# Performance work log

Measured on AMD Instinct MI355X. Metric: run time of the kernel, lower is better.

## Reference

```python
import math
import jax, jax.numpy as jnp
import numpy as np

B, S, D, H = 2, 2048, 1024, 16
HD = D // H  # 64


def setup_inputs() -> dict:
    key = jax.random.key(0)
    k0, k1, k2, k3, k4 = jax.random.split(key, 5)
    x = jax.random.normal(k0, (B, S, D), dtype=jnp.float32)
    # standard RoPE angles: rotations[s, i] = (cos(s*theta_i), sin(s*theta_i))
    inv_freq = 1.0 / (10000.0 ** (jnp.arange(0, HD, 2, dtype=jnp.float32) / HD))  # [HD/2]
    ang = jnp.arange(S, dtype=jnp.float32)[:, None] * inv_freq[None, :]           # [S, HD/2]
    rotations = jnp.stack([jnp.cos(ang), jnp.sin(ang)], axis=-1)                  # [S, HD/2, 2]
    scale = D ** -0.5
    w_qkv = jax.random.normal(k1, (3 * D, D), dtype=jnp.float32) * scale
    b_qkv = jax.random.normal(k2, (3 * D,), dtype=jnp.float32) * 0.01
    w_o = jax.random.normal(k3, (D, D), dtype=jnp.float32) * scale
    b_o = jax.random.normal(k4, (D,), dtype=jnp.float32) * 0.01
    return {"input": x, "rotations": rotations, "w_qkv": w_qkv, "b_qkv": b_qkv,
            "w_o": w_o, "b_o": b_o}


def _apply_rotary(t, cos, sin):
    # t: [B, H, S, HD]; cos/sin: [S, HD/2] broadcast over B,H
    te, to = t[..., 0::2], t[..., 1::2]
    re = te * cos - to * sin
    ro = te * sin + to * cos
    return jnp.stack([re, ro], axis=-1).reshape(t.shape)


def reference(input, rotations, w_qkv, b_qkv, w_o, b_o):
    Bx, Sx, Dx = input.shape
    qkv = input @ w_qkv.T + b_qkv                      # [B, S, 3D]
    q, k, v = jnp.split(qkv, 3, axis=-1)
    def to_heads(t):
        return t.reshape(Bx, Sx, H, HD).transpose(0, 2, 1, 3)  # [B, H, S, HD]
    q, k, v = to_heads(q), to_heads(k), to_heads(v)
    cos, sin = rotations[..., 0], rotations[..., 1]    # [S, HD/2]
    q = _apply_rotary(q, cos, sin)
    k = _apply_rotary(k, cos, sin)
    scale = math.sqrt(1.0 / float(HD))
    scores = jnp.einsum('bhsd,bhtd->bhst', q * scale, k)  # [B, H, S, S]
    w = jax.nn.softmax(scores.astype(jnp.float32), axis=-1).astype(scores.dtype)
    attn = jnp.einsum('bhst,bhtd->bhsd', w, v)          # [B, H, S, HD]
    attn = attn.transpose(0, 2, 1, 3).reshape(Bx, Sx, Dx)
    return attn @ w_o.T + b_o
```

## Files before the change

kernel.cpp:

```cpp
#include <hip/hip_runtime.h>

typedef __bf16 bf16_t;
typedef __bf16 bf16x8 __attribute__((ext_vector_type(8)));
typedef __bf16 bf16x4 __attribute__((ext_vector_type(4)));
typedef __bf16 bf16x2 __attribute__((ext_vector_type(2)));
typedef float f32x4 __attribute__((ext_vector_type(4)));
typedef float f32x16 __attribute__((ext_vector_type(16)));

#define B_ 2
#define S_ 2048
#define D_ 1024
#define H_ 16
#define HD_ 64

#define MFMA(a, b, c) __builtin_amdgcn_mfma_f32_16x16x32_bf16(a, b, c, 0, 0, 0)
#define MFMA32(a, b, c) __builtin_amdgcn_mfma_f32_32x32x16_bf16(a, b, c, 0, 0, 0)

static __device__ __forceinline__ bf16x8 ldb8(const bf16_t* p) {
    return *(const bf16x8*)p;
}

static __device__ __forceinline__ void gload16(const void* g, void* l) {
    __builtin_amdgcn_global_load_lds((const __attribute__((address_space(1))) void*)g,
                                     (__attribute__((address_space(3))) void*)l, 16, 0, 0);
}

static __device__ __forceinline__ unsigned cvtpk(float a, float b) {
    union { bf16x2 h; unsigned u; } cv;
    cv.h[0] = (bf16_t)a;
    cv.h[1] = (bf16_t)b;
    return cv.u;
}
static __device__ __forceinline__ float xhalf_max(float x) {
    return fmaxf(x, __shfl_xor(x, 32));
}

__global__ __launch_bounds__(256) void k_cvt(const float* __restrict__ in,
                                             bf16_t* __restrict__ out, int n4) {
    int i = blockIdx.x * 256 + threadIdx.x;
    int stride = gridDim.x * 256;
    for (; i < n4; i += stride) {
        float4 v = ((const float4*)in)[i];
        bf16x4 o;
        o[0] = (bf16_t)v.x; o[1] = (bf16_t)v.y; o[2] = (bf16_t)v.z; o[3] = (bf16_t)v.w;
        ((bf16x4*)out)[i] = o;
    }
}

static __device__ __forceinline__ void gemm_core(const bf16_t* __restrict__ A,
                                                 const bf16_t* __restrict__ Bt,
                                                 const int K, bf16_t* ldsA, bf16_t* ldsB,
                                                 f32x4 acc[4][4]) {
    const int tid = threadIdx.x;
    const int wave = tid >> 6, lane = tid & 63;
    const int g = lane >> 4, q16 = lane & 15;
    const int wm = wave >> 1, wn = wave & 1;
    const int mb = blockIdx.x * 128, nb = blockIdx.y * 128;
    const int r0 = lane >> 2, c8 = (lane & 3) * 8;

#pragma unroll
    for (int i = 0; i < 4; ++i)
#pragma unroll
        for (int j = 0; j < 4; ++j) {
            f32x4 z = {0.f, 0.f, 0.f, 0.f};
            acc[i][j] = z;
        }

    const bf16_t* ga0 = A + (size_t)(mb + wave * 16 + r0) * K + c8;
    const bf16_t* ga1 = A + (size_t)(mb + 64 + wave * 16 + r0) * K + c8;
    const bf16_t* gb0 = Bt + (size_t)(nb + wave * 16 + r0) * K + c8;
    const bf16_t* gb1 = Bt + (size_t)(nb + 64 + wave * 16 + r0) * K + c8;
    bf16_t* la0 = ldsA + (wave * 16) * 32;
    bf16_t* la1 = ldsA + (64 + wave * 16) * 32;
    bf16_t* lb0 = ldsB + (wave * 16) * 32;
    bf16_t* lb1 = ldsB + (64 + wave * 16) * 32;

    for (int k0 = 0; k0 < K; k0 += 32) {
        gload16(ga0 + k0, la0);
        gload16(ga1 + k0, la1);
        gload16(gb0 + k0, lb0);
        gload16(gb1 + k0, lb1);
        __syncthreads();
        bf16x8 af[4], bfv[4];
#pragma unroll
        for (int i = 0; i < 4; ++i)
            af[i] = ldb8(ldsA + (wm * 64 + i * 16 + q16) * 32 + 8 * g);
#pragma unroll
        for (int j = 0; j < 4; ++j)
            bfv[j] = ldb8(ldsB + (wn * 64 + j * 16 + q16) * 32 + 8 * g);
#pragma unroll
        for (int i = 0; i < 4; ++i)
#pragma unroll
            for (int j = 0; j < 4; ++j)
                acc[i][j] = MFMA(af[i], bfv[j], acc[i][j]);
        __syncthreads();
    }
}

__global__ __launch_bounds__(256) void k_gemm_qkv(const bf16_t* __restrict__ xb,
                                                  const bf16_t* __restrict__ wqb,
                                                  const float* __restrict__ bqkv,
                                                  const float* __restrict__ rot,
                                                  bf16_t* __restrict__ qa,
                                                  bf16_t* __restrict__ kt,
                                                  bf16_t* __restrict__ vt) {
    __shared__ bf16_t ldsA[128 * 32];
    __shared__ bf16_t ldsB[128 * 32];
    f32x4 acc[4][4];
    gemm_core(xb, wqb, 1024, ldsA, ldsB, acc);

    const int tid = threadIdx.x;
    const int wave = tid >> 6, lane = tid & 63;
    const int g = lane >> 4, q16 = lane & 15;
    const int wm = wave >> 1, wn = wave & 1;
    const int mb = blockIdx.x * 128, nb = blockIdx.y * 128;
    const int third = nb >> 10;
    const float QS = 0.125f * 1.44269504088896f;

    if (third < 2) {
        const float2* cs2 = (const float2*)rot;
#pragma unroll
        for (int j = 0; j < 4; ++j) {
            int n = nb + wn * 64 + j * 16 + q16;
            float bias = bqkv[n];
            int d = n & 1023;
            int h = d >> 6, hd = d & 63;
            int i2 = hd >> 1;
            bool odd = (hd & 1) != 0;
#pragma unroll
            for (int i = 0; i < 4; ++i) {
                int m0 = mb + wm * 64 + i * 16 + 4 * g;
#pragma unroll
                for (int r = 0; r < 4; ++r) {
                    int mm = m0 + r;
                    int s = mm & 2047, b = mm >> 11;
                    float val = acc[i][j][r] + bias;
                    float prt = __shfl_xor(val, 1);
                    float2 cs = cs2[s * 32 + i2];
                    float rv = val * cs.x + (odd ? prt * cs.y : -(prt * cs.y));
                    size_t base = (size_t)(b * H_ + h) * (S_ * 64);
                    if (third == 0) {
                        qa[base + (size_t)s * HD_ + hd] = (bf16_t)(rv * QS);
                    } else {
                        int idx = ((s >> 5) << 11) + ((hd >> 4) << 9) + ((s & 31) << 4)
                                + (((hd >> 3) & 1) << 3) + (hd & 7);
                        kt[base + idx] = (bf16_t)rv;
                    }
                }
            }
        }
    } else {
#pragma unroll
        for (int j = 0; j < 4; ++j) {
            int n = nb + wn * 64 + j * 16 + q16;
            float bias = bqkv[n];
            int d = n & 1023;
            int h = d >> 6, hd = d & 63;
#pragma unroll
            for (int i = 0; i < 4; ++i) {
                int m0 = mb + wm * 64 + i * 16 + 4 * g;
                int s0 = m0 & 2047, b = m0 >> 11;
                bf16x4 pk;
#pragma unroll
                for (int r = 0; r < 4; ++r) pk[r] = (bf16_t)(acc[i][j][r] + bias);
                int x = (((s0 >> 4) & 1) << 1) + (hd >> 5);
                size_t base = (size_t)(b * H_ + h) * (S_ * 64);
                size_t idx = ((size_t)(s0 >> 5) << 11) + (x << 9) + ((hd & 31) << 4)
                           + (((s0 >> 3) & 1) << 3) + (s0 & 7);
                *(bf16x4*)(vt + base + idx) = pk;
            }
        }
    }
}

static __device__ __forceinline__ void loadK(const bf16_t* kbase, bf16x8 (&kf)[4]) {
#pragma unroll
    for (int j = 0; j < 4; ++j) kf[j] = ldb8(kbase + 512 * j);
}
static __device__ __forceinline__ void loadV(const bf16_t* vbase, bf16x8 (&vf)[4]) {
    vf[0] = ldb8(vbase);
    vf[1] = ldb8(vbase + 512);
    vf[2] = ldb8(vbase + 1024);
    vf[3] = ldb8(vbase + 1536);
}

static __device__ __forceinline__ f32x16 qk4(const bf16x8 (&kf)[4], const bf16x8 (&qf)[4]) {
    f32x16 s = {0.f, 0.f, 0.f, 0.f, 0.f, 0.f, 0.f, 0.f,
                0.f, 0.f, 0.f, 0.f, 0.f, 0.f, 0.f, 0.f};
    __builtin_amdgcn_s_setprio(1);
#pragma unroll
    for (int j = 0; j < 4; ++j) s = MFMA32(kf[j], qf[j], s);
    __builtin_amdgcn_s_setprio(0);
    return s;
}

static __device__ __forceinline__ void softmax_pa(f32x16& s, float& m, float& lsum,
                                                  f32x16& o0, f32x16& o1,
                                                  int hi, bf16x8& pa0v, bf16x8& pa1v) {
    float a0 = fmaxf(fmaxf(s[0], s[1]), s[2]);
    float a1 = fmaxf(fmaxf(s[3], s[4]), s[5]);
    float a2 = fmaxf(fmaxf(s[6], s[7]), s[8]);
    float a3 = fmaxf(fmaxf(s[9], s[10]), s[11]);
    float a4 = fmaxf(fmaxf(s[12], s[13]), s[14]);
    float tm = fmaxf(fmaxf(fmaxf(a0, a1), a2), fmaxf(fmaxf(a3, a4), s[15]));
    tm = xhalf_max(tm);

    bool ok = (tm <= m + 8.0f);
    if (!__all(ok)) {
        float mn = fmaxf(m, tm);
        float ce = __builtin_amdgcn_exp2f(m - mn);
        m = mn;
        lsum *= ce;
#pragma unroll
        for (int r = 0; r < 16; ++r) {
            int q = (r & 3) + 8 * (r >> 2) + 4 * hi;
            float c = __shfl(ce, q);
            o0[r] *= c; o1[r] *= c;
        }
    }

#pragma unroll
    for (int r = 0; r < 16; ++r) s[r] = __builtin_amdgcn_exp2f(s[r] - m);
    float ps = (((s[0] + s[1]) + (s[2] + s[3])) + ((s[4] + s[5]) + (s[6] + s[7])))
             + (((s[8] + s[9]) + (s[10] + s[11])) + ((s[12] + s[13]) + (s[14] + s[15])));
    lsum += ps;

    unsigned c0 = cvtpk(s[0], s[1]),   c1 = cvtpk(s[2], s[3]);
    unsigned c2 = cvtpk(s[4], s[5]),   c3 = cvtpk(s[6], s[7]);
    unsigned d0 = cvtpk(s[8], s[9]),   d1 = cvtpk(s[10], s[11]);
    unsigned d2 = cvtpk(s[12], s[13]), d3 = cvtpk(s[14], s[15]);
    unsigned x0 = __shfl_xor(c0, 32), x1 = __shfl_xor(c1, 32);
    unsigned x2 = __shfl_xor(c2, 32), x3 = __shfl_xor(c3, 32);
    unsigned y0 = __shfl_xor(d0, 32), y1 = __shfl_xor(d1, 32);
    unsigned y2 = __shfl_xor(d2, 32), y3 = __shfl_xor(d3, 32);

    union { unsigned u[4]; bf16x8 v; } pa0, pa1;
    pa0.u[0] = hi ? x2 : c0;
    pa0.u[1] = hi ? x3 : c1;
    pa0.u[2] = hi ? c2 : x0;
    pa0.u[3] = hi ? c3 : x1;
    pa1.u[0] = hi ? y2 : d0;
    pa1.u[1] = hi ? y3 : d1;
    pa1.u[2] = hi ? d2 : y0;
    pa1.u[3] = hi ? d3 : y1;
    pa0v = pa0.v;
    pa1v = pa1.v;
}

static __device__ __forceinline__ void pv4(const bf16x8 pa0, const bf16x8 pa1,
                                           const bf16x8 (&vf)[4], f32x16& o0, f32x16& o1) {
    __builtin_amdgcn_s_setprio(1);
    o0 = MFMA32(pa0, vf[0], o0);
    o1 = MFMA32(pa0, vf[1], o1);
    o0 = MFMA32(pa1, vf[2], o0);
    o1 = MFMA32(pa1, vf[3], o1);
    __builtin_amdgcn_s_setprio(0);
}

__global__ __launch_bounds__(256, 4) void k_attn(const bf16_t* __restrict__ qa,
                                                 const bf16_t* __restrict__ kt,
                                                 const bf16_t* __restrict__ vt,
                                                 bf16_t* __restrict__ attn) {
    __shared__ float lm[2][32];
    __shared__ float ll[2][32];
    __shared__ float lo[2][2][16][64];
    const int tid = threadIdx.x;
    const int wave = tid >> 6, lane = tid & 63;
    const int l31 = lane & 31, hi = lane >> 5;
    const int pair = wave & 1;
    const int thalf = wave >> 1;
    const int bh = blockIdx.y;
    const int q0 = blockIdx.x * 64 + pair * 32;

    const bf16_t* Qp = qa + ((size_t)bh * S_ + q0) * HD_;
    const int laneoff = (2 * l31 + hi) * 8;
    const bf16_t* kl = kt + (size_t)bh * (S_ * 64) + (size_t)thalf * 65536 + laneoff;
    const bf16_t* vl = vt + (size_t)bh * (S_ * 64) + (size_t)thalf * 65536 + laneoff;

    bf16x8 qf[4];
    const bf16_t* qptr = Qp + l31 * HD_ + 8 * hi;
#pragma unroll
    for (int j = 0; j < 4; ++j) qf[j] = ldb8(qptr + 16 * j);

    f32x16 o0 = {0.f, 0.f, 0.f, 0.f, 0.f, 0.f, 0.f, 0.f,
                 0.f, 0.f, 0.f, 0.f, 0.f, 0.f, 0.f, 0.f};
    f32x16 o1 = o0;
    float m = -1e30f, lsum = 0.f;

    bf16x8 kE[4], kO[4];
    loadK(kl, kE);

    for (int i = 0; i < 16; ++i) {
        {
            f32x16 s = qk4(kE, qf);
            loadK(kl + 2048, kO);
            bf16x8 vv[4];
            loadV(vl, vv);
            bf16x8 pa0, pa1;
            softmax_pa(s, m, lsum, o0, o1, hi, pa0, pa1);
            pv4(pa0, pa1, vv, o0, o1);
        }
        {
            f32x16 s = qk4(kO, qf);
            loadK(kl + 4096, kE);
            bf16x8 vv[4];
            loadV(vl + 2048, vv);
            bf16x8 pa0, pa1;
            softmax_pa(s, m, lsum, o0, o1, hi, pa0, pa1);
            pv4(pa0, pa1, vv, o0, o1);
        }
        kl += 4096;
        vl += 4096;
    }

    float lfull = lsum + __shfl_xor(lsum, 32);
    if (thalf) {
        if (!hi) {
            lm[pair][l31] = m;
            ll[pair][l31] = lfull;
        }
#pragma unroll
        for (int r = 0; r < 16; ++r) {
            lo[pair][0][r][lane] = o0[r];
            lo[pair][1][r][lane] = o1[r];
        }
    }
    __syncthreads();
    if (!thalf) {
        float mb_ = lm[pair][l31];
        float lb_ = ll[pair][l31];
        float ms = fmaxf(m, mb_);
        float ca = __builtin_amdgcn_exp2f(m - ms);
        float cb = __builtin_amdgcn_exp2f(mb_ - ms);
        float invL = 1.0f / (lfull * ca + lb_ * cb);
        const int b = bh >> 4, h = bh & 15;
        bf16_t* op = attn + ((size_t)b * S_ + q0) * D_ + h * HD_;
#pragma unroll
        for (int r = 0; r < 16; ++r) {
            int q = (r & 3) + 8 * (r >> 2) + 4 * hi;
            float caq = __shfl(ca, q);
            float cbq = __shfl(cb, q);
            float invq = __shfl(invL, q);
            float O0 = (o0[r] * caq + lo[pair][0][r][lane] * cbq) * invq;
            float O1 = (o1[r] * caq + lo[pair][1][r][lane] * cbq) * invq;
            op[(size_t)q * D_ + l31] = (bf16_t)O0;
            op[(size_t)q * D_ + 32 + l31] = (bf16_t)O1;
        }
    }
}

__global__ __launch_bounds__(256) void k_gemm_out(const bf16_t* __restrict__ attn,
                                                  const bf16_t* __restrict__ wob,
                                                  const float* __restrict__ bo,
                                                  float* __restrict__ out) {
    __shared__ bf16_t ldsA[128 * 32];
    __shared__ bf16_t ldsB[128 * 32];
    f32x4 acc[4][4];
    gemm_core(attn, wob, 1024, ldsA, ldsB, acc);

    const int tid = threadIdx.x;
    const int wave = tid >> 6, lane = tid & 63;
    const int g = lane >> 4, q16 = lane & 15;
    const int wm = wave >> 1, wn = wave & 1;
    const int mb = blockIdx.x * 128, nb = blockIdx.y * 128;
#pragma unroll
    for (int j = 0; j < 4; ++j) {
        int n = nb + wn * 64 + j * 16 + q16;
        float bias = bo[n];
#pragma unroll
        for (int i = 0; i < 4; ++i) {
            int m0 = mb + wm * 64 + i * 16 + 4 * g;
#pragma unroll
            for (int r = 0; r < 4; ++r)
                out[(size_t)(m0 + r) * D_ + n] = acc[i][j][r] + bias;
        }
    }
}

extern "C" void kernel_launch(void* const* d_in, const int* in_sizes, int n_in,
                              void* d_out, int out_size, void* d_ws, size_t ws_size,
                              hipStream_t stream) {
    const float* x    = (const float*)d_in[0];
    const float* rot  = (const float*)d_in[1];
    const float* wqkv = (const float*)d_in[2];
    const float* bqkv = (const float*)d_in[3];
    const float* wo   = (const float*)d_in[4];
    const float* bo   = (const float*)d_in[5];
    float* out = (float*)d_out;

    char* ws = (char*)d_ws;
    bf16_t* xb   = (bf16_t*)(ws);
    bf16_t* wqb  = (bf16_t*)(ws + ((size_t)8 << 20));
    bf16_t* wob  = (bf16_t*)(ws + ((size_t)14 << 20));
    bf16_t* qa   = (bf16_t*)(ws + ((size_t)16 << 20));
    bf16_t* kt   = (bf16_t*)(ws + ((size_t)24 << 20));
    bf16_t* vt   = (bf16_t*)(ws + ((size_t)32 << 20));
    bf16_t* attn = (bf16_t*)(ws + ((size_t)40 << 20));

    k_cvt<<<1024, 256, 0, stream>>>(x, xb, (B_ * S_ * D_) / 4);
    k_cvt<<<1024, 256, 0, stream>>>(wqkv, wqb, (3 * D_ * D_) / 4);
    k_cvt<<<1024, 256, 0, stream>>>(wo, wob, (D_ * D_) / 4);
    k_gemm_qkv<<<dim3(32, 24), 256, 0, stream>>>(xb, wqb, bqkv, rot, qa, kt, vt);
    k_attn<<<dim3(32, 32), 256, 0, stream>>>(qa, kt, vt, attn);
    k_gemm_out<<<dim3(32, 8), 256, 0, stream>>>(attn, wob, bo, out);
}
```

Before: 221.5 us.

## Merge conversion kernels and transpose Q/K GEMM for vectorized RoPE epilogue

The three fp32-to-bf16 conversion launches are merged into one kernel that picks its source buffer by index range, which removes two launches. For the Q and K sections of the QKV projection, the GEMM operands are swapped so each lane's accumulator holds four consecutive head-dim values for one token. RoPE rotation pairs therefore sit in the same lane, which removes the cross-lane shuffles and allows vectorized bias, rotation and bf16x4 stores in place of scalar scattered stores. The risks are extra branching in the conversion loop and a different GEMM memory access pattern for the swapped operands.

```diff
diff --git a/kernel.cpp b/kernel.cpp
--- a/kernel.cpp
+++ b/kernel.cpp
@@ -35,27 +35,43 @@
     return fmaxf(x, __shfl_xor(x, 32));
 }
 
-__global__ __launch_bounds__(256) void k_cvt(const float* __restrict__ in,
-                                             bf16_t* __restrict__ out, int n4) {
+#define N4_X  1048576
+#define N4_WQ 786432
+#define N4_WO 262144
+__global__ __launch_bounds__(256) void k_cvt3(const float* __restrict__ x,
+                                              const float* __restrict__ wq,
+                                              const float* __restrict__ wo,
+                                              bf16_t* __restrict__ xb,
+                                              bf16_t* __restrict__ wqb,
+                                              bf16_t* __restrict__ wob) {
     int i = blockIdx.x * 256 + threadIdx.x;
     int stride = gridDim.x * 256;
-    for (; i < n4; i += stride) {
-        float4 v = ((const float4*)in)[i];
+    for (; i < N4_X + N4_WQ + N4_WO; i += stride) {
+        const float4* src;
+        bf16x4* dst;
+        int off;
+        if (i < N4_X) {
+            src = (const float4*)x; dst = (bf16x4*)xb; off = i;
+        } else if (i < N4_X + N4_WQ) {
+            src = (const float4*)wq; dst = (bf16x4*)wqb; off = i - N4_X;
+        } else {
+            src = (const float4*)wo; dst = (bf16x4*)wob; off = i - (N4_X + N4_WQ);
+        }
+        float4 v = src[off];
         bf16x4 o;
         o[0] = (bf16_t)v.x; o[1] = (bf16_t)v.y; o[2] = (bf16_t)v.z; o[3] = (bf16_t)v.w;
-        ((bf16x4*)out)[i] = o;
+        dst[off] = o;
     }
 }
 
 static __device__ __forceinline__ void gemm_core(const bf16_t* __restrict__ A,
                                                  const bf16_t* __restrict__ Bt,
                                                  const int K, bf16_t* ldsA, bf16_t* ldsB,
-                                                 f32x4 acc[4][4]) {
+                                                 f32x4 acc[4][4], int mb, int nb) {
     const int tid = threadIdx.x;
     const int wave = tid >> 6, lane = tid & 63;
     const int g = lane >> 4, q16 = lane & 15;
     const int wm = wave >> 1, wn = wave & 1;
-    const int mb = blockIdx.x * 128, nb = blockIdx.y * 128;
     const int r0 = lane >> 2, c8 = (lane & 3) * 8;
 
 #pragma unroll
@@ -106,59 +122,58 @@
                                                   bf16_t* __restrict__ vt) {
     __shared__ bf16_t ldsA[128 * 32];
     __shared__ bf16_t ldsB[128 * 32];
-    f32x4 acc[4][4];
-    gemm_core(xb, wqb, 1024, ldsA, ldsB, acc);
-
     const int tid = threadIdx.x;
     const int wave = tid >> 6, lane = tid & 63;
     const int g = lane >> 4, q16 = lane & 15;
     const int wm = wave >> 1, wn = wave & 1;
-    const int mb = blockIdx.x * 128, nb = blockIdx.y * 128;
-    const int third = nb >> 10;
+    const int sx = blockIdx.x;
+    const int third = blockIdx.y >> 3;
+    const int ny = blockIdx.y & 7;
     const float QS = 0.125f * 1.44269504088896f;
+    f32x4 acc[4][4];
 
     if (third < 2) {
-        const float2* cs2 = (const float2*)rot;
+        gemm_core(wqb, xb, 1024, ldsA, ldsB, acc, third * 1024 + ny * 128, sx * 128);
+        const int h = ny * 2 + wm;
+#pragma unroll
+        for (int i = 0; i < 4; ++i) {
+            const int hdb = i * 16 + 4 * g;
+            float4 bi = *(const float4*)&bqkv[third * 1024 + ny * 128 + wm * 64 + hdb];
+#pragma unroll
+            for (int j = 0; j < 4; ++j) {
+                int mm = sx * 128 + wn * 64 + j * 16 + q16;
+                int s = mm & 2047, b = mm >> 11;
+                float4 cs = *(const float4*)&rot[s * 64 + hdb];
+                float v0 = acc[i][j][0] + bi.x, v1 = acc[i][j][1] + bi.y;
+                float v2 = acc[i][j][2] + bi.z, v3 = acc[i][j][3] + bi.w;
+                float r0 = v0 * cs.x - v1 * cs.y, r1 = v0 * cs.y + v1 * cs.x;
+                float r2 = v2 * cs.z - v3 * cs.w, r3 = v2 * cs.w + v3 * cs.z;
+                size_t base = (size_t)(b * H_ + h) * (S_ * 64);
+                bf16x4 pk;
+                if (third == 0) {
+                    pk[0] = (bf16_t)(r0 * QS); pk[1] = (bf16_t)(r1 * QS);
+                    pk[2] = (bf16_t)(r2 * QS); pk[3] = (bf16_t)(r3 * QS);
+                    *(bf16x4*)(qa + base + (size_t)s * HD_ + hdb) = pk;
+                } else {
+                    pk[0] = (bf16_t)r0; pk[1] = (bf16_t)r1;
+                    pk[2] = (bf16_t)r2; pk[3] = (bf16_t)r3;
+                    size_t idx = ((size_t)(s >> 5) << 11) + (i << 9) + ((s & 31) << 4)
+                               + ((g >> 1) << 3) + ((g & 1) << 2);
+                    *(bf16x4*)(kt + base + idx) = pk;
+                }
+            }
+        }
+    } else {
+        gemm_core(xb, wqb, 1024, ldsA, ldsB, acc, sx * 128, 2048 + ny * 128);
 #pragma unroll
         for (int j = 0; j < 4; ++j) {
-            int n = nb + wn * 64 + j * 16 + q16;
+            int n = 2048 + ny * 128 + wn * 64 + j * 16 + q16;
             float bias = bqkv[n];
             int d = n & 1023;
             int h = d >> 6, hd = d & 63;
-            int i2 = hd >> 1;
-            bool odd = (hd & 1) != 0;
 #pragma unroll
             for (int i = 0; i < 4; ++i) {
-                int m0 = mb + wm * 64 + i * 16 + 4 * g;
-#pragma unroll
-                for (int r = 0; r < 4; ++r) {
-                    int mm = m0 + r;
-                    int s = mm & 2047, b = mm >> 11;
-                    float val = acc[i][j][r] + bias;
-                    float prt = __shfl_xor(val, 1);
-                    float2 cs = cs2[s * 32 + i2];
-                    float rv = val * cs.x + (odd ? prt * cs.y : -(prt * cs.y));
-                    size_t base = (size_t)(b * H_ + h) * (S_ * 64);
-                    if (third == 0) {
-                        qa[base + (size_t)s * HD_ + hd] = (bf16_t)(rv * QS);
-                    } else {
-                        int idx = ((s >> 5) << 11) + ((hd >> 4) << 9) + ((s & 31) << 4)
-                                + (((hd >> 3) & 1) << 3) + (hd & 7);
-                        kt[base + idx] = (bf16_t)rv;
-                    }
-                }
-            }
-        }
-    } else {
-#pragma unroll
-        for (int j = 0; j < 4; ++j) {
-            int n = nb + wn * 64 + j * 16 + q16;
-            float bias = bqkv[n];
-            int d = n & 1023;
-            int h = d >> 6, hd = d & 63;
-#pragma unroll
-            for (int i = 0; i < 4; ++i) {
-                int m0 = mb + wm * 64 + i * 16 + 4 * g;
+                int m0 = sx * 128 + wm * 64 + i * 16 + 4 * g;
                 int s0 = m0 & 2047, b = m0 >> 11;
                 bf16x4 pk;
 #pragma unroll
@@ -356,7 +371,7 @@
     __shared__ bf16_t ldsA[128 * 32];
     __shared__ bf16_t ldsB[128 * 32];
     f32x4 acc[4][4];
-    gemm_core(attn, wob, 1024, ldsA, ldsB, acc);
+    gemm_core(attn, wob, 1024, ldsA, ldsB, acc, blockIdx.x * 128, blockIdx.y * 128);
 
     const int tid = threadIdx.x;
     const int wave = tid >> 6, lane = tid & 63;
@@ -397,9 +412,7 @@
     bf16_t* vt   = (bf16_t*)(ws + ((size_t)32 << 20));
     bf16_t* attn = (bf16_t*)(ws + ((size_t)40 << 20));
 
-    k_cvt<<<1024, 256, 0, stream>>>(x, xb, (B_ * S_ * D_) / 4);
-    k_cvt<<<1024, 256, 0, stream>>>(wqkv, wqb, (3 * D_ * D_) / 4);
-    k_cvt<<<1024, 256, 0, stream>>>(wo, wob, (D_ * D_) / 4);
+    k_cvt3<<<2048, 256, 0, stream>>>(x, wqkv, wo, xb, wqb, wob);
     k_gemm_qkv<<<dim3(32, 24), 256, 0, stream>>>(xb, wqb, bqkv, rot, qa, kt, vt);
     k_attn<<<dim3(32, 32), 256, 0, stream>>>(qa, kt, vt, attn);
     k_gemm_out<<<dim3(32, 8), 256, 0, stream>>>(attn, wob, bo, out);
```

Measured after the change: 202.0 us. 8.8% less time.
